# Kernel optimization log

Hardware: AMD Instinct MI355X
Metric: run time of the kernel (lower is better)

The kernel has to match this reference:

```python
import jax, jax.numpy as jnp
import numpy as np

EPS = 1e-5
B, C, H, W, K = 16, 512, 64, 64, 32


def setup_inputs() -> dict:
    key = jax.random.key(0)
    ks = jax.random.split(key, 6)
    std = 1.0 / float(np.sqrt(K * C))
    return {
        "x": jax.random.normal(ks[0], (B, C, H, W), jnp.float32),
        "conv_w": jax.random.normal(ks[1], (C, C), jnp.float32) * (1.0 / np.sqrt(C)),
        "bn2_g": jnp.ones((C,), jnp.float32),
        "bn2_b": jnp.zeros((C,), jnp.float32),
        "bn2_m": jnp.zeros((C,), jnp.float32),
        "bn2_v": jnp.ones((C,), jnp.float32),
        "codewords": jax.random.uniform(ks[2], (K, C), jnp.float32, -std, std),
        "scale": jax.random.uniform(ks[3], (K,), jnp.float32, -1.0, 0.0),
        "bn1_g": jnp.ones((K,), jnp.float32),
        "bn1_b": jnp.zeros((K,), jnp.float32),
        "bn1_m": jnp.zeros((K,), jnp.float32),
        "bn1_v": jnp.ones((K,), jnp.float32),
        "fc_w": jax.random.normal(ks[4], (C, C), jnp.float32) * (1.0 / np.sqrt(C)),
        "fc_b": jnp.zeros((C,), jnp.float32),
    }


def reference(x, conv_w, bn2_g, bn2_b, bn2_m, bn2_v, codewords, scale,
              bn1_g, bn1_b, bn1_m, bn1_v, fc_w, fc_b):
    b, c, h, w = x.shape
    k = codewords.shape[0]
    # encoding_project: 1x1 conv (no bias) + BatchNorm2d (inference) + ReLU
    proj = jnp.einsum('oc,bchw->bohw', conv_w, x)
    s2 = (jax.lax.rsqrt(bn2_v + EPS) * bn2_g)[None, :, None, None]
    proj = jax.nn.relu((proj - bn2_m[None, :, None, None]) * s2 + bn2_b[None, :, None, None])
    # Encoding: scaled-L2 softmax assignment + residual aggregation
    feats = proj.reshape(b, c, h * w).transpose(0, 2, 1)          # (B, N, C)
    x2 = jnp.sum(feats * feats, axis=-1)                          # (B, N)
    c2 = jnp.sum(codewords * codewords, axis=-1)                  # (K,)
    xc = jnp.einsum('bnc,kc->bnk', feats, codewords)              # (B, N, K)
    dist = scale[None, None, :] * (x2[..., None] - 2.0 * xc + c2[None, None, :])
    assign = jax.nn.softmax(dist, axis=2)                         # (B, N, K)
    # sum_n w[b,n,k] * (x[b,n,c] - c[k,c])  without materializing (B,N,K,C)
    encoded = (jnp.einsum('bnk,bnc->bkc', assign, feats)
               - jnp.einsum('bnk,kc->bkc', assign, codewords))    # (B, K, C)
    # BatchNorm1d over num_codes (inference) + ReLU
    s1 = (jax.lax.rsqrt(bn1_v + EPS) * bn1_g)[None, :, None]
    encoded = jax.nn.relu((encoded - bn1_m[None, :, None]) * s1 + bn1_b[None, :, None])
    encoding_feat = jnp.mean(encoded, axis=1)                     # (B, C)
    # fc -> sigmoid gate, residual relu
    gamma = jax.nn.sigmoid(encoding_feat @ fc_w.T + fc_b)         # (B, C)
    output = jax.nn.relu(x + x * gamma[:, :, None, None])
    return (encoding_feat, output)
```

## Files before the change

### kernel.cpp

```cpp
#include <hip/hip_runtime.h>
#include <hip/hip_bf16.h>

#define BB   16
#define CC   512
#define HWN  4096
#define KK   32
#define EPSF 1e-5f

typedef short bf16x8 __attribute__((ext_vector_type(8)));
typedef float f32x4  __attribute__((ext_vector_type(4)));

#define MFMA16 __builtin_amdgcn_mfma_f32_16x16x32_bf16

#define GLD16(g, l) __builtin_amdgcn_global_load_lds(                          \
    (const __attribute__((address_space(1))) void*)(g),                        \
    (__attribute__((address_space(3))) void*)(l), 16, 0, 0)

static __device__ __forceinline__ unsigned short f2b(float f) {
    unsigned u = __builtin_bit_cast(unsigned, f);
    unsigned r = (u + 0x7FFFu + ((u >> 16) & 1u)) >> 16;
    return (unsigned short)r;
}

__global__ __launch_bounds__(256) void k_prep(const float* __restrict__ W,
                                              const float* __restrict__ cw,
                                              const float* __restrict__ scale,
                                              const float* __restrict__ g1,
                                              const float* __restrict__ b1,
                                              const float* __restrict__ m1,
                                              const float* __restrict__ v1,
                                              unsigned short* __restrict__ Wb,
                                              unsigned short* __restrict__ cwb,
                                              float* __restrict__ sc2,
                                              float* __restrict__ s1,
                                              float* __restrict__ t1) {
    int bid = blockIdx.x, t = threadIdx.x;
    if (bid < 256) {
        int i = (bid * 256 + t) * 4;
        float4 v = *(const float4*)(W + i);
        uint2 p;
        p.x = (unsigned)f2b(v.x) | ((unsigned)f2b(v.y) << 16);
        p.y = (unsigned)f2b(v.z) | ((unsigned)f2b(v.w) << 16);
        *(uint2*)(Wb + i) = p;
    } else if (bid < 272) {
        int i = ((bid - 256) * 256 + t) * 4;
        float4 v = *(const float4*)(cw + i);
        uint2 p;
        p.x = (unsigned)f2b(v.x) | ((unsigned)f2b(v.y) << 16);
        p.y = (unsigned)f2b(v.z) | ((unsigned)f2b(v.w) << 16);
        *(uint2*)(cwb + i) = p;
    } else {
        int k = t >> 3, l8 = t & 7;
        const float* row = cw + k * CC + l8 * 64;
        float s = 0.f;
#pragma unroll
        for (int i = 0; i < 16; i++) {
            float4 c4 = *(const float4*)(row + i * 4);
            s += c4.x * c4.x + c4.y * c4.y + c4.z * c4.z + c4.w * c4.w;
        }
        s += __shfl_xor(s, 1); s += __shfl_xor(s, 2); s += __shfl_xor(s, 4);
        if (l8 == 0) sc2[k] = scale[k] * s;
        if (t < KK) {
            float sv = rsqrtf(v1[t] + EPSF) * g1[t];
            s1[t] = sv;
            t1[t] = b1[t] - m1[t] * sv;
        }
    }
}

__global__ __launch_bounds__(256) void k_transpose(const float* __restrict__ x,
                                                   unsigned short* __restrict__ xT) {
    __shared__ float tile[64][65];
    int bid = blockIdx.x;
    int b   = bid >> 9;
    int rem = bid & 511;
    int c0  = (rem >> 6) * 64;
    int n0  = (rem & 63) * 64;
    int t = threadIdx.x;
#pragma unroll
    for (int p = 0; p < 4; p++) {
        int s = p * 256 + t;
        int row = s >> 4, col = (s & 15) * 4;
        float4 v = *(const float4*)(x + (size_t)(b * CC + c0 + row) * HWN + n0 + col);
        tile[row][col]     = v.x;
        tile[row][col + 1] = v.y;
        tile[row][col + 2] = v.z;
        tile[row][col + 3] = v.w;
    }
    __syncthreads();
    int nr = t >> 2;
    int cg = (t & 3) * 16;
    unsigned u[8];
#pragma unroll
    for (int j = 0; j < 8; j++) {
        u[j] = (unsigned)f2b(tile[cg + 2 * j][nr]) |
               ((unsigned)f2b(tile[cg + 2 * j + 1][nr]) << 16);
    }
    unsigned short* dst = xT + (size_t)(b * HWN + n0 + nr) * CC + c0 + cg;
    uint4 a; a.x = u[0]; a.y = u[1]; a.z = u[2]; a.w = u[3];
    uint4 c; c.x = u[4]; c.y = u[5]; c.z = u[6]; c.w = u[7];
    *(uint4*)(dst)     = a;
    *(uint4*)(dst + 8) = c;
}

__global__ __launch_bounds__(256) void k_conv_gemm(const unsigned short* __restrict__ xT,
                                                   const unsigned short* __restrict__ Wb,
                                                   const float* __restrict__ g2,
                                                   const float* __restrict__ b2,
                                                   const float* __restrict__ m2,
                                                   const float* __restrict__ v2,
                                                   unsigned short* __restrict__ feats,
                                                   unsigned short* __restrict__ featsT,
                                                   float* __restrict__ x2) {
    __shared__ short As[128 * 32];
    __shared__ short Bs[128 * 32];
    int bid = blockIdx.x;
    int b   = bid >> 7;
    int rem = bid & 127;
    int m0  = (rem >> 2) * 128;
    int o0  = (rem & 3) * 128;
    int t = threadIdx.x, lane = t & 63, wave = t >> 6;
    int mb = (wave >> 1) * 64, ob = (wave & 1) * 64;
    int col_l = lane & 15, quad = lane >> 4;

    f32x4 zero = {0.f, 0.f, 0.f, 0.f};
    f32x4 acc[4][4];
#pragma unroll
    for (int i = 0; i < 4; i++)
#pragma unroll
        for (int j = 0; j < 4; j++) acc[i][j] = zero;

    const unsigned short* Abase = xT + (size_t)(b * HWN + m0) * CC;
    const unsigned short* Bbase = Wb + (size_t)o0 * CC;

    for (int kc = 0; kc < 16; kc++) {
        int k0 = kc * 32;
#pragma unroll
        for (int p = 0; p < 2; p++) {
            int sbase = p * 256 + wave * 64;
            int s = sbase + lane;
            const unsigned short* ga = Abase + (size_t)(s >> 2) * CC + k0 + (s & 3) * 8;
            const unsigned short* gb = Bbase + (size_t)(s >> 2) * CC + k0 + (s & 3) * 8;
            GLD16(ga, (char*)As + sbase * 16);
            GLD16(gb, (char*)Bs + sbase * 16);
        }
        __syncthreads();
        bf16x8 af[4], bfv[4];
#pragma unroll
        for (int im = 0; im < 4; im++)
            af[im] = *(const bf16x8*)(&As[(mb + im * 16 + col_l) * 32 + quad * 8]);
#pragma unroll
        for (int in = 0; in < 4; in++)
            bfv[in] = *(const bf16x8*)(&Bs[(ob + in * 16 + col_l) * 32 + quad * 8]);
#pragma unroll
        for (int im = 0; im < 4; im++)
#pragma unroll
            for (int in = 0; in < 4; in++)
                acc[im][in] = MFMA16(af[im], bfv[in], acc[im][in], 0, 0, 0);
        __syncthreads();
    }

    float scv[4], offv[4];
    int oidx[4];
#pragma unroll
    for (int in = 0; in < 4; in++) {
        int o = o0 + ob + in * 16 + col_l;
        oidx[in] = o;
        float sv = rsqrtf(v2[o] + EPSF) * g2[o];
        scv[in]  = sv;
        offv[in] = b2[o] - m2[o] * sv;
    }
#pragma unroll
    for (int im = 0; im < 4; im++) {
        int nb = m0 + mb + im * 16 + quad * 4;
        float v[4][4];
#pragma unroll
        for (int in = 0; in < 4; in++)
#pragma unroll
            for (int r = 0; r < 4; r++)
                v[in][r] = fmaxf(acc[im][in][r] * scv[in] + offv[in], 0.f);
#pragma unroll
        for (int r = 0; r < 4; r++) {
            unsigned short* frow = feats + (size_t)(b * HWN + nb + r) * CC;
#pragma unroll
            for (int in = 0; in < 4; in++) frow[oidx[in]] = f2b(v[in][r]);
        }
#pragma unroll
        for (int in = 0; in < 4; in++) {
            uint2 pk;
            pk.x = (unsigned)f2b(v[in][0]) | ((unsigned)f2b(v[in][1]) << 16);
            pk.y = (unsigned)f2b(v[in][2]) | ((unsigned)f2b(v[in][3]) << 16);
            *(uint2*)(featsT + (size_t)(b * CC + oidx[in]) * HWN + nb) = pk;
        }
#pragma unroll
        for (int r = 0; r < 4; r++) {
            float ss = v[0][r] * v[0][r] + v[1][r] * v[1][r] +
                       v[2][r] * v[2][r] + v[3][r] * v[3][r];
            ss += __shfl_xor(ss, 1); ss += __shfl_xor(ss, 2);
            ss += __shfl_xor(ss, 4); ss += __shfl_xor(ss, 8);
            if (col_l == 0) atomicAdd(&x2[b * HWN + nb + r], ss);
        }
    }
}

__global__ __launch_bounds__(256) void k_assign(const unsigned short* __restrict__ feats,
                                                const unsigned short* __restrict__ cwb,
                                                const float* __restrict__ x2,
                                                const float* __restrict__ scale,
                                                const float* __restrict__ sc2,
                                                unsigned short* __restrict__ assignT,
                                                float* __restrict__ asum) {
    __shared__ short cwl[32 * 520];
    __shared__ short fl[256 * 32];
    __shared__ float sl[KK], cl[KK];
    int bid = blockIdx.x;
    int b = bid >> 4, n0 = (bid & 15) * 256;
    int t = threadIdx.x, lane = t & 63, wave = t >> 6;
    int col_l = lane & 15, quad = lane >> 4;

#pragma unroll
    for (int p = 0; p < 8; p++) {
        int s = p * 256 + t;
        int row = s >> 6, c8 = (s & 63) * 8;
        *(uint4*)(&cwl[row * 520 + c8]) = *(const uint4*)(cwb + row * 512 + c8);
    }
    if (t < KK) { sl[t] = scale[t]; cl[t] = sc2[t]; }

    f32x4 zero = {0.f, 0.f, 0.f, 0.f};
    f32x4 acc[2][4];
#pragma unroll
    for (int i = 0; i < 2; i++)
#pragma unroll
        for (int j = 0; j < 4; j++) acc[i][j] = zero;

    const unsigned short* Fbase = feats + (size_t)(b * HWN + n0) * CC;
    for (int ci = 0; ci < 16; ci++) {
        int c0 = ci * 32;
#pragma unroll
        for (int p = 0; p < 4; p++) {
            int sbase = p * 256 + wave * 64;
            int s = sbase + lane;
            const unsigned short* gp = Fbase + (size_t)(s >> 2) * CC + c0 + (s & 3) * 8;
            GLD16(gp, (char*)fl + sbase * 16);
        }
        __syncthreads();
        bf16x8 af0 = *(const bf16x8*)(&cwl[(col_l) * 520 + c0 + quad * 8]);
        bf16x8 af1 = *(const bf16x8*)(&cwl[(16 + col_l) * 520 + c0 + quad * 8]);
#pragma unroll
        for (int ct = 0; ct < 4; ct++) {
            bf16x8 bf = *(const bf16x8*)(&fl[(wave * 64 + ct * 16 + col_l) * 32 + quad * 8]);
            acc[0][ct] = MFMA16(af0, bf, acc[0][ct], 0, 0, 0);
            acc[1][ct] = MFMA16(af1, bf, acc[1][ct], 0, 0, 0);
        }
        __syncthreads();
    }

    float asw[2][4];
#pragma unroll
    for (int mk = 0; mk < 2; mk++)
#pragma unroll
        for (int r = 0; r < 4; r++) asw[mk][r] = 0.f;

#pragma unroll
    for (int ct = 0; ct < 4; ct++) {
        int n = n0 + wave * 64 + ct * 16 + col_l;
        float x2v = x2[b * HWN + n];
        float d[2][4];
        float mmax = -3.4e38f;
#pragma unroll
        for (int mk = 0; mk < 2; mk++)
#pragma unroll
            for (int r = 0; r < 4; r++) {
                int k = mk * 16 + quad * 4 + r;
                d[mk][r] = sl[k] * (x2v - 2.f * acc[mk][ct][r]) + cl[k];
                mmax = fmaxf(mmax, d[mk][r]);
            }
        mmax = fmaxf(mmax, __shfl_xor(mmax, 16));
        mmax = fmaxf(mmax, __shfl_xor(mmax, 32));
        float ssum = 0.f;
#pragma unroll
        for (int mk = 0; mk < 2; mk++)
#pragma unroll
            for (int r = 0; r < 4; r++) {
                d[mk][r] = __expf(d[mk][r] - mmax);
                ssum += d[mk][r];
            }
        ssum += __shfl_xor(ssum, 16);
        ssum += __shfl_xor(ssum, 32);
        float rinv = 1.f / ssum;
#pragma unroll
        for (int mk = 0; mk < 2; mk++)
#pragma unroll
            for (int r = 0; r < 4; r++) {
                int k = mk * 16 + quad * 4 + r;
                float a = d[mk][r] * rinv;
                assignT[(size_t)(b * KK + k) * HWN + n] = f2b(a);
                float p = a;
                p += __shfl_xor(p, 1); p += __shfl_xor(p, 2);
                p += __shfl_xor(p, 4); p += __shfl_xor(p, 8);
                asw[mk][r] += p;
            }
    }
#pragma unroll
    for (int mk = 0; mk < 2; mk++)
#pragma unroll
        for (int r = 0; r < 4; r++)
            if (col_l == 0)
                atomicAdd(&asum[b * KK + mk * 16 + quad * 4 + r], asw[mk][r]);
}

__global__ __launch_bounds__(256) void k_encode(const unsigned short* __restrict__ featsT,
                                                const unsigned short* __restrict__ assignT,
                                                float* __restrict__ enc) {
    __shared__ short Al[128 * 32];
    __shared__ short Bl[32 * 32];
    int bid = blockIdx.x;
    int b   = bid >> 5;
    int rem = bid & 31;
    int c0  = (rem >> 3) * 128;
    int ns  = rem & 7;
    int t = threadIdx.x, lane = t & 63, wave = t >> 6;
    int col_l = lane & 15, quad = lane >> 4;

    f32x4 zero = {0.f, 0.f, 0.f, 0.f};
    f32x4 acc[2][2];
    acc[0][0] = zero; acc[0][1] = zero; acc[1][0] = zero; acc[1][1] = zero;

    const unsigned short* Abase = featsT + (size_t)(b * CC + c0) * HWN;
    const unsigned short* Bbase = assignT + (size_t)(b * KK) * HWN;

    for (int it = 0; it < 16; it++) {
        int n0 = ns * 512 + it * 32;
#pragma unroll
        for (int p = 0; p < 2; p++) {
            int sbase = p * 256 + wave * 64;
            int s = sbase + lane;
            const unsigned short* gp = Abase + (size_t)(s >> 2) * HWN + n0 + (s & 3) * 8;
            GLD16(gp, (char*)Al + sbase * 16);
        }
        if (wave < 2) {
            int sbase = wave * 64;
            int s = sbase + lane;
            const unsigned short* gp = Bbase + (size_t)(s >> 2) * HWN + n0 + (s & 3) * 8;
            GLD16(gp, (char*)Bl + sbase * 16);
        }
        __syncthreads();
        bf16x8 a0 = *(const bf16x8*)(&Al[(wave * 32 + col_l) * 32 + quad * 8]);
        bf16x8 a1 = *(const bf16x8*)(&Al[(wave * 32 + 16 + col_l) * 32 + quad * 8]);
        bf16x8 b0 = *(const bf16x8*)(&Bl[(col_l) * 32 + quad * 8]);
        bf16x8 b1 = *(const bf16x8*)(&Bl[(16 + col_l) * 32 + quad * 8]);
        acc[0][0] = MFMA16(a0, b0, acc[0][0], 0, 0, 0);
        acc[0][1] = MFMA16(a0, b1, acc[0][1], 0, 0, 0);
        acc[1][0] = MFMA16(a1, b0, acc[1][0], 0, 0, 0);
        acc[1][1] = MFMA16(a1, b1, acc[1][1], 0, 0, 0);
        __syncthreads();
    }
#pragma unroll
    for (int i2 = 0; i2 < 2; i2++)
#pragma unroll
        for (int ck = 0; ck < 2; ck++)
#pragma unroll
            for (int r = 0; r < 4; r++) {
                int c = c0 + wave * 32 + i2 * 16 + quad * 4 + r;
                int k = ck * 16 + col_l;
                atomicAdd(&enc[(size_t)(b * CC + c) * KK + k], acc[i2][ck][r]);
            }
}

__global__ __launch_bounds__(256) void k_efeat(const float* __restrict__ enc,
                                               const float* __restrict__ asum,
                                               const float* __restrict__ cwf,
                                               const float* __restrict__ s1,
                                               const float* __restrict__ t1,
                                               float* __restrict__ efeat) {
    __shared__ float asl[KK], s1l[KK], t1l[KK];
    int b = blockIdx.x, t = threadIdx.x;
    if (t < KK) { asl[t] = asum[b * KK + t]; s1l[t] = s1[t]; t1l[t] = t1[t]; }
    __syncthreads();
#pragma unroll
    for (int cc = 0; cc < 2; cc++) {
        int c = cc * 256 + t;
        const float* er = enc + (size_t)(b * CC + c) * KK;
        float s = 0.f;
#pragma unroll
        for (int k = 0; k < KK; k++) {
            float v = (er[k] - asl[k] * cwf[k * CC + c]) * s1l[k] + t1l[k];
            s += fmaxf(v, 0.f);
        }
        efeat[b * CC + c] = s * (1.f / 32.f);
    }
}

__global__ __launch_bounds__(256) void k_fc(const float* __restrict__ efeat,
                                            const float* __restrict__ fcw,
                                            const float* __restrict__ fcb,
                                            float* __restrict__ gamma) {
    __shared__ float ef[CC];
    int bid = blockIdx.x;
    int b  = bid >> 1;
    int o0 = (bid & 1) * 256;
    int t = threadIdx.x;
    if (t < 128) *(float4*)(&ef[t * 4]) = *(const float4*)(efeat + b * CC + t * 4);
    __syncthreads();
    int o = o0 + t;
    float a = fcb[o];
    const float* wrow = fcw + (size_t)o * CC;
#pragma unroll 4
    for (int c4 = 0; c4 < 128; c4++) {
        float4 w = *(const float4*)(wrow + c4 * 4);
        float4 e = *(const float4*)(&ef[c4 * 4]);
        a += w.x * e.x + w.y * e.y + w.z * e.z + w.w * e.w;
    }
    gamma[b * CC + o] = 1.f / (1.f + __expf(-a));
}

__global__ __launch_bounds__(256) void k_gate(const float* __restrict__ x,
                                              const float* __restrict__ gamma,
                                              float* __restrict__ out) {
    int i = blockIdx.x * 256 + threadIdx.x;
    int idx = i * 4;
    int b = idx >> 21;
    int c = (idx >> 12) & 511;
    float g = 1.f + gamma[b * CC + c];
    float4 v = *(const float4*)(x + idx);
    v.x = fmaxf(v.x * g, 0.f);
    v.y = fmaxf(v.y * g, 0.f);
    v.z = fmaxf(v.z * g, 0.f);
    v.w = fmaxf(v.w * g, 0.f);
    *(float4*)(out + idx) = v;
}

extern "C" void kernel_launch(void* const* d_in, const int* in_sizes, int n_in,
                              void* d_out, int out_size, void* d_ws, size_t ws_size,
                              hipStream_t stream) {
    const float* x      = (const float*)d_in[0];
    const float* conv_w = (const float*)d_in[1];
    const float* bn2_g  = (const float*)d_in[2];
    const float* bn2_b  = (const float*)d_in[3];
    const float* bn2_m  = (const float*)d_in[4];
    const float* bn2_v  = (const float*)d_in[5];
    const float* cw     = (const float*)d_in[6];
    const float* scale  = (const float*)d_in[7];
    const float* bn1_g  = (const float*)d_in[8];
    const float* bn1_b  = (const float*)d_in[9];
    const float* bn1_m  = (const float*)d_in[10];
    const float* bn1_v  = (const float*)d_in[11];
    const float* fc_w   = (const float*)d_in[12];
    const float* fc_b   = (const float*)d_in[13];

    float* outf = (float*)d_out;
    char* ws = (char*)d_ws;

    unsigned short* feats   = (unsigned short*)(ws);
    unsigned short* assignT = (unsigned short*)(ws + 67108864);
    unsigned short* Wb      = (unsigned short*)(ws + 71303168);
    unsigned short* cwb     = (unsigned short*)(ws + 71827456);
    float*          x2      = (float*)(ws + 71860224);
    float*          asum    = (float*)(ws + 72122368);
    float*          enc     = (float*)(ws + 72124416);
    float*          sc2     = (float*)(ws + 73172992);
    float*          s1      = (float*)(ws + 73173248);
    float*          t1      = (float*)(ws + 73173504);
    float*          gamma   = (float*)(ws + 73173760);

    unsigned short* xT     = (unsigned short*)((char*)d_out + 32768);
    unsigned short* featsT = (unsigned short*)((char*)d_out + 67141632);

    hipMemsetAsync(x2, 0, 262144 + 2048 + 1048576, stream);

    k_prep<<<273, 256, 0, stream>>>(conv_w, cw, scale, bn1_g, bn1_b, bn1_m, bn1_v,
                                    Wb, cwb, sc2, s1, t1);
    k_transpose<<<8192, 256, 0, stream>>>(x, xT);
    k_conv_gemm<<<2048, 256, 0, stream>>>(xT, Wb, bn2_g, bn2_b, bn2_m, bn2_v,
                                          feats, featsT, x2);
    k_assign<<<256, 256, 0, stream>>>(feats, cwb, x2, scale, sc2, assignT, asum);
    k_encode<<<512, 256, 0, stream>>>(featsT, assignT, enc);
    k_efeat<<<16, 256, 0, stream>>>(enc, asum, cw, s1, t1, outf);
    k_fc<<<32, 256, 0, stream>>>(outf, fc_w, fc_b, gamma);
    k_gate<<<32768, 256, 0, stream>>>(x, gamma, outf + 8192);
}
```

Before: 450.6 us.

## Stage conv epilogue through swizzled LDS, deepen K chunks, retile assign/encode/gate

The conv GEMM epilogue now writes bf16 results into an XOR-swizzled LDS tile, then emits coalesced 16-byte stores for both feats and featsT, replacing scattered 2-byte and 8-byte global stores. Its K loop and k_encode's N loop load two 32-wide panels per barrier, halving the number of syncs. k_assign uses 128-row tiles with twice as many blocks to raise occupancy, and k_gate processes one channel row per block with a single gamma load. The changes cost extra LDS traffic and a barrier in the epilogue, and the scalar LDS gathers for feats may cause bank conflicts.

After: 442.7 us. About the same (-1.8%).

```diff
diff --git a/kernel.cpp b/kernel.cpp
--- a/kernel.cpp
+++ b/kernel.cpp
@@ -15,6 +15,8 @@
 #define GLD16(g, l) __builtin_amdgcn_global_load_lds(                          \
     (const __attribute__((address_space(1))) void*)(g),                        \
     (__attribute__((address_space(3))) void*)(l), 16, 0, 0)
+
+#define EADDR(o, n) ((o) * 136 + (((((n) >> 3) ^ (((o) >> 3) & 15))) << 3) + ((n) & 7))
 
 static __device__ __forceinline__ unsigned short f2b(float f) {
     unsigned u = __builtin_bit_cast(unsigned, f);
@@ -112,8 +114,7 @@
                                                    unsigned short* __restrict__ feats,
                                                    unsigned short* __restrict__ featsT,
                                                    float* __restrict__ x2) {
-    __shared__ short As[128 * 32];
-    __shared__ short Bs[128 * 32];
+    __shared__ __align__(16) short lds[17408];
     int bid = blockIdx.x;
     int b   = bid >> 7;
     int rem = bid & 127;
@@ -133,73 +134,96 @@
     const unsigned short* Abase = xT + (size_t)(b * HWN + m0) * CC;
     const unsigned short* Bbase = Wb + (size_t)o0 * CC;
 
-    for (int kc = 0; kc < 16; kc++) {
-        int k0 = kc * 32;
-#pragma unroll
-        for (int p = 0; p < 2; p++) {
-            int sbase = p * 256 + wave * 64;
-            int s = sbase + lane;
-            const unsigned short* ga = Abase + (size_t)(s >> 2) * CC + k0 + (s & 3) * 8;
-            const unsigned short* gb = Bbase + (size_t)(s >> 2) * CC + k0 + (s & 3) * 8;
-            GLD16(ga, (char*)As + sbase * 16);
-            GLD16(gb, (char*)Bs + sbase * 16);
+    for (int kc = 0; kc < 8; kc++) {
+        int c0 = kc * 64;
+#pragma unroll
+        for (int pc = 0; pc < 2; pc++) {
+#pragma unroll
+            for (int p = 0; p < 2; p++) {
+                int sbase = p * 256 + wave * 64;
+                int s = sbase + lane;
+                int row = s >> 2, part = (s & 3) * 8;
+                GLD16(Abase + (size_t)row * CC + c0 + pc * 32 + part,
+                      (char*)lds + pc * 8192 + sbase * 16);
+                GLD16(Bbase + (size_t)row * CC + c0 + pc * 32 + part,
+                      (char*)lds + 16384 + pc * 8192 + sbase * 16);
+            }
         }
         __syncthreads();
-        bf16x8 af[4], bfv[4];
-#pragma unroll
-        for (int im = 0; im < 4; im++)
-            af[im] = *(const bf16x8*)(&As[(mb + im * 16 + col_l) * 32 + quad * 8]);
-#pragma unroll
-        for (int in = 0; in < 4; in++)
-            bfv[in] = *(const bf16x8*)(&Bs[(ob + in * 16 + col_l) * 32 + quad * 8]);
-#pragma unroll
-        for (int im = 0; im < 4; im++)
+#pragma unroll
+        for (int pc = 0; pc < 2; pc++) {
+            bf16x8 af[4], bfv[4];
+#pragma unroll
+            for (int im = 0; im < 4; im++)
+                af[im] = *(const bf16x8*)(&lds[pc * 4096 + (mb + im * 16 + col_l) * 32 + quad * 8]);
 #pragma unroll
             for (int in = 0; in < 4; in++)
-                acc[im][in] = MFMA16(af[im], bfv[in], acc[im][in], 0, 0, 0);
+                bfv[in] = *(const bf16x8*)(&lds[8192 + pc * 4096 + (ob + in * 16 + col_l) * 32 + quad * 8]);
+#pragma unroll
+            for (int im = 0; im < 4; im++)
+#pragma unroll
+                for (int in = 0; in < 4; in++)
+                    acc[im][in] = MFMA16(af[im], bfv[in], acc[im][in], 0, 0, 0);
+        }
         __syncthreads();
     }
 
     float scv[4], offv[4];
-    int oidx[4];
 #pragma unroll
     for (int in = 0; in < 4; in++) {
         int o = o0 + ob + in * 16 + col_l;
-        oidx[in] = o;
         float sv = rsqrtf(v2[o] + EPSF) * g2[o];
         scv[in]  = sv;
         offv[in] = b2[o] - m2[o] * sv;
     }
 #pragma unroll
     for (int im = 0; im < 4; im++) {
-        int nb = m0 + mb + im * 16 + quad * 4;
-        float v[4][4];
+        int n_l = mb + im * 16 + quad * 4;
+        float vv[4][4];
 #pragma unroll
         for (int in = 0; in < 4; in++)
 #pragma unroll
             for (int r = 0; r < 4; r++)
-                v[in][r] = fmaxf(acc[im][in][r] * scv[in] + offv[in], 0.f);
+                vv[in][r] = fmaxf(acc[im][in][r] * scv[in] + offv[in], 0.f);
+#pragma unroll
+        for (int in = 0; in < 4; in++) {
+            int o_l = ob + in * 16 + col_l;
+            uint2 pk;
+            pk.x = (unsigned)f2b(vv[in][0]) | ((unsigned)f2b(vv[in][1]) << 16);
+            pk.y = (unsigned)f2b(vv[in][2]) | ((unsigned)f2b(vv[in][3]) << 16);
+            *(uint2*)(&lds[EADDR(o_l, n_l)]) = pk;
+        }
 #pragma unroll
         for (int r = 0; r < 4; r++) {
-            unsigned short* frow = feats + (size_t)(b * HWN + nb + r) * CC;
-#pragma unroll
-            for (int in = 0; in < 4; in++) frow[oidx[in]] = f2b(v[in][r]);
-        }
-#pragma unroll
-        for (int in = 0; in < 4; in++) {
-            uint2 pk;
-            pk.x = (unsigned)f2b(v[in][0]) | ((unsigned)f2b(v[in][1]) << 16);
-            pk.y = (unsigned)f2b(v[in][2]) | ((unsigned)f2b(v[in][3]) << 16);
-            *(uint2*)(featsT + (size_t)(b * CC + oidx[in]) * HWN + nb) = pk;
-        }
-#pragma unroll
-        for (int r = 0; r < 4; r++) {
-            float ss = v[0][r] * v[0][r] + v[1][r] * v[1][r] +
-                       v[2][r] * v[2][r] + v[3][r] * v[3][r];
+            float ss = vv[0][r] * vv[0][r] + vv[1][r] * vv[1][r] +
+                       vv[2][r] * vv[2][r] + vv[3][r] * vv[3][r];
             ss += __shfl_xor(ss, 1); ss += __shfl_xor(ss, 2);
             ss += __shfl_xor(ss, 4); ss += __shfl_xor(ss, 8);
-            if (col_l == 0) atomicAdd(&x2[b * HWN + nb + r], ss);
-        }
+            if (col_l == 0) atomicAdd(&x2[b * HWN + m0 + n_l + r], ss);
+        }
+    }
+    __syncthreads();
+
+#pragma unroll
+    for (int rr = 0; rr < 8; rr++) {
+        int o = rr * 16 + (t >> 4);
+        int n16 = t & 15;
+        uint4 v = *(const uint4*)(&lds[EADDR(o, n16 * 8)]);
+        *(uint4*)(featsT + (size_t)(b * CC + o0 + o) * HWN + m0 + n16 * 8) = v;
+    }
+#pragma unroll
+    for (int rr = 0; rr < 8; rr++) {
+        int n = rr * 16 + (t >> 4);
+        int o16 = t & 15;
+        unsigned u[4];
+#pragma unroll
+        for (int jj = 0; jj < 4; jj++) {
+            unsigned short a = lds[EADDR(o16 * 8 + 2 * jj,     n)];
+            unsigned short bsh = lds[EADDR(o16 * 8 + 2 * jj + 1, n)];
+            u[jj] = (unsigned)a | ((unsigned)bsh << 16);
+        }
+        uint4 pk; pk.x = u[0]; pk.y = u[1]; pk.z = u[2]; pk.w = u[3];
+        *(uint4*)(feats + (size_t)(b * HWN + m0 + n) * CC + o0 + o16 * 8) = pk;
     }
 }
 
@@ -211,10 +235,10 @@
                                                 unsigned short* __restrict__ assignT,
                                                 float* __restrict__ asum) {
     __shared__ short cwl[32 * 520];
-    __shared__ short fl[256 * 32];
+    __shared__ short fl[128 * 32];
     __shared__ float sl[KK], cl[KK];
     int bid = blockIdx.x;
-    int b = bid >> 4, n0 = (bid & 15) * 256;
+    int b = bid >> 5, n0 = (bid & 31) * 128;
     int t = threadIdx.x, lane = t & 63, wave = t >> 6;
     int col_l = lane & 15, quad = lane >> 4;
 
@@ -227,28 +251,25 @@
     if (t < KK) { sl[t] = scale[t]; cl[t] = sc2[t]; }
 
     f32x4 zero = {0.f, 0.f, 0.f, 0.f};
-    f32x4 acc[2][4];
-#pragma unroll
-    for (int i = 0; i < 2; i++)
-#pragma unroll
-        for (int j = 0; j < 4; j++) acc[i][j] = zero;
+    f32x4 acc[2][2];
+    acc[0][0] = zero; acc[0][1] = zero; acc[1][0] = zero; acc[1][1] = zero;
 
     const unsigned short* Fbase = feats + (size_t)(b * HWN + n0) * CC;
     for (int ci = 0; ci < 16; ci++) {
         int c0 = ci * 32;
 #pragma unroll
-        for (int p = 0; p < 4; p++) {
+        for (int p = 0; p < 2; p++) {
             int sbase = p * 256 + wave * 64;
             int s = sbase + lane;
-            const unsigned short* gp = Fbase + (size_t)(s >> 2) * CC + c0 + (s & 3) * 8;
-            GLD16(gp, (char*)fl + sbase * 16);
+            GLD16(Fbase + (size_t)(s >> 2) * CC + c0 + (s & 3) * 8,
+                  (char*)fl + sbase * 16);
         }
         __syncthreads();
         bf16x8 af0 = *(const bf16x8*)(&cwl[(col_l) * 520 + c0 + quad * 8]);
         bf16x8 af1 = *(const bf16x8*)(&cwl[(16 + col_l) * 520 + c0 + quad * 8]);
 #pragma unroll
-        for (int ct = 0; ct < 4; ct++) {
-            bf16x8 bf = *(const bf16x8*)(&fl[(wave * 64 + ct * 16 + col_l) * 32 + quad * 8]);
+        for (int ct = 0; ct < 2; ct++) {
+            bf16x8 bf = *(const bf16x8*)(&fl[(wave * 32 + ct * 16 + col_l) * 32 + quad * 8]);
             acc[0][ct] = MFMA16(af0, bf, acc[0][ct], 0, 0, 0);
             acc[1][ct] = MFMA16(af1, bf, acc[1][ct], 0, 0, 0);
         }
@@ -262,8 +283,8 @@
         for (int r = 0; r < 4; r++) asw[mk][r] = 0.f;
 
 #pragma unroll
-    for (int ct = 0; ct < 4; ct++) {
-        int n = n0 + wave * 64 + ct * 16 + col_l;
+    for (int ct = 0; ct < 2; ct++) {
+        int n = n0 + wave * 32 + ct * 16 + col_l;
         float x2v = x2[b * HWN + n];
         float d[2][4];
         float mmax = -3.4e38f;
@@ -312,8 +333,8 @@
 __global__ __launch_bounds__(256) void k_encode(const unsigned short* __restrict__ featsT,
                                                 const unsigned short* __restrict__ assignT,
                                                 float* __restrict__ enc) {
-    __shared__ short Al[128 * 32];
-    __shared__ short Bl[32 * 32];
+    __shared__ short Al[2][128 * 32];
+    __shared__ short Bl[2][32 * 32];
     int bid = blockIdx.x;
     int b   = bid >> 5;
     int rem = bid & 31;
@@ -329,30 +350,37 @@
     const unsigned short* Abase = featsT + (size_t)(b * CC + c0) * HWN;
     const unsigned short* Bbase = assignT + (size_t)(b * KK) * HWN;
 
-    for (int it = 0; it < 16; it++) {
-        int n0 = ns * 512 + it * 32;
-#pragma unroll
-        for (int p = 0; p < 2; p++) {
-            int sbase = p * 256 + wave * 64;
-            int s = sbase + lane;
-            const unsigned short* gp = Abase + (size_t)(s >> 2) * HWN + n0 + (s & 3) * 8;
-            GLD16(gp, (char*)Al + sbase * 16);
-        }
-        if (wave < 2) {
-            int sbase = wave * 64;
-            int s = sbase + lane;
-            const unsigned short* gp = Bbase + (size_t)(s >> 2) * HWN + n0 + (s & 3) * 8;
-            GLD16(gp, (char*)Bl + sbase * 16);
+    for (int it = 0; it < 8; it++) {
+        int n0 = ns * 512 + it * 64;
+#pragma unroll
+        for (int pc = 0; pc < 2; pc++) {
+#pragma unroll
+            for (int p = 0; p < 2; p++) {
+                int sbase = p * 256 + wave * 64;
+                int s = sbase + lane;
+                GLD16(Abase + (size_t)(s >> 2) * HWN + n0 + pc * 32 + (s & 3) * 8,
+                      (char*)Al[pc] + sbase * 16);
+            }
+        }
+        {
+            int s = t;
+            int pan = s >> 7, row = (s & 127) >> 2, part = (s & 3) * 8;
+            GLD16(Bbase + (size_t)row * HWN + n0 + pan * 32 + part,
+                  (char*)Bl[0] + ((wave >> 1) * 2048 + (wave & 1) * 1024) + lane * 16);
+            (void)pan;
         }
         __syncthreads();
-        bf16x8 a0 = *(const bf16x8*)(&Al[(wave * 32 + col_l) * 32 + quad * 8]);
-        bf16x8 a1 = *(const bf16x8*)(&Al[(wave * 32 + 16 + col_l) * 32 + quad * 8]);
-        bf16x8 b0 = *(const bf16x8*)(&Bl[(col_l) * 32 + quad * 8]);
-        bf16x8 b1 = *(const bf16x8*)(&Bl[(16 + col_l) * 32 + quad * 8]);
-        acc[0][0] = MFMA16(a0, b0, acc[0][0], 0, 0, 0);
-        acc[0][1] = MFMA16(a0, b1, acc[0][1], 0, 0, 0);
-        acc[1][0] = MFMA16(a1, b0, acc[1][0], 0, 0, 0);
-        acc[1][1] = MFMA16(a1, b1, acc[1][1], 0, 0, 0);
+#pragma unroll
+        for (int pc = 0; pc < 2; pc++) {
+            bf16x8 a0 = *(const bf16x8*)(&Al[pc][(wave * 32 + col_l) * 32 + quad * 8]);
+            bf16x8 a1 = *(const bf16x8*)(&Al[pc][(wave * 32 + 16 + col_l) * 32 + quad * 8]);
+            bf16x8 b0 = *(const bf16x8*)(&Bl[pc][(col_l) * 32 + quad * 8]);
+            bf16x8 b1 = *(const bf16x8*)(&Bl[pc][(16 + col_l) * 32 + quad * 8]);
+            acc[0][0] = MFMA16(a0, b0, acc[0][0], 0, 0, 0);
+            acc[0][1] = MFMA16(a0, b1, acc[0][1], 0, 0, 0);
+            acc[1][0] = MFMA16(a1, b0, acc[1][0], 0, 0, 0);
+            acc[1][1] = MFMA16(a1, b1, acc[1][1], 0, 0, 0);
+        }
         __syncthreads();
     }
 #pragma unroll
@@ -417,17 +445,20 @@
 __global__ __launch_bounds__(256) void k_gate(const float* __restrict__ x,
                                               const float* __restrict__ gamma,
                                               float* __restrict__ out) {
-    int i = blockIdx.x * 256 + threadIdx.x;
-    int idx = i * 4;
-    int b = idx >> 21;
-    int c = (idx >> 12) & 511;
-    float g = 1.f + gamma[b * CC + c];
-    float4 v = *(const float4*)(x + idx);
-    v.x = fmaxf(v.x * g, 0.f);
-    v.y = fmaxf(v.y * g, 0.f);
-    v.z = fmaxf(v.z * g, 0.f);
-    v.w = fmaxf(v.w * g, 0.f);
-    *(float4*)(out + idx) = v;
+    int bid = blockIdx.x;
+    float g = 1.f + gamma[bid];
+    const float* xr = x + ((size_t)bid << 12);
+    float* orow = out + ((size_t)bid << 12);
+    int t4 = threadIdx.x * 4;
+#pragma unroll
+    for (int u = 0; u < 4; u++) {
+        float4 v = *(const float4*)(xr + u * 1024 + t4);
+        v.x = fmaxf(v.x * g, 0.f);
+        v.y = fmaxf(v.y * g, 0.f);
+        v.z = fmaxf(v.z * g, 0.f);
+        v.w = fmaxf(v.w * g, 0.f);
+        *(float4*)(orow + u * 1024 + t4) = v;
+    }
 }
 
 extern "C" void kernel_launch(void* const* d_in, const int* in_sizes, int n_in,
@@ -473,9 +504,9 @@
     k_transpose<<<8192, 256, 0, stream>>>(x, xT);
     k_conv_gemm<<<2048, 256, 0, stream>>>(xT, Wb, bn2_g, bn2_b, bn2_m, bn2_v,
                                           feats, featsT, x2);
-    k_assign<<<256, 256, 0, stream>>>(feats, cwb, x2, scale, sc2, assignT, asum);
+    k_assign<<<512, 256, 0, stream>>>(feats, cwb, x2, scale, sc2, assignT, asum);
     k_encode<<<512, 256, 0, stream>>>(featsT, assignT, enc);
     k_efeat<<<16, 256, 0, stream>>>(enc, asum, cw, s1, t1, outf);
     k_fc<<<32, 256, 0, stream>>>(outf, fc_w, fc_b, gamma);
-    k_gate<<<32768, 256, 0, stream>>>(x, gamma, outf + 8192);
-}
+    k_gate<<<8192, 256, 0, stream>>>(x, gamma, outf + 8192);
+}
```
